# Kernel tuning notes

Hardware: AMD Instinct MI355X
Metric: run time of the kernel (lower is better)

Reference implementation:

```python
import jax, jax.numpy as jnp
import numpy as np

B, A, F, H = 64, 128, 32, 64


def setup_inputs() -> dict:
    key = jax.random.key(0)
    ks = jax.random.split(key, 16)
    def dense(k, fan_in, fan_out):
        return jax.random.normal(k, (fan_in, fan_out), jnp.float32) / np.sqrt(fan_in)
    inp = {
        "X": jax.random.normal(ks[0], (B, A, F), jnp.float32),
        "mask": jax.random.randint(ks[1], (B, A), 0, 2, jnp.int32),
        # base MLP: F -> H -> H -> 1
        "base_W1": dense(ks[2], F, H), "base_b1": jnp.zeros((H,), jnp.float32),
        "base_W2": dense(ks[3], H, H), "base_b2": jnp.zeros((H,), jnp.float32),
        "base_W3": dense(ks[4], H, 1), "base_b3": jnp.zeros((1,), jnp.float32),
        # pair MLP: 2F -> H -> H -> 1
        "pair_W1": dense(ks[5], 2 * F, H), "pair_b1": jnp.zeros((H,), jnp.float32),
        "pair_W2": dense(ks[6], H, H), "pair_b2": jnp.zeros((H,), jnp.float32),
        "pair_W3": dense(ks[7], H, 1), "pair_b3": jnp.zeros((1,), jnp.float32),
    }
    return inp


def reference(X, mask, base_W1, base_b1, base_W2, base_b2, base_W3, base_b3,
              pair_W1, pair_b1, pair_W2, pair_b2, pair_W3, pair_b3):
    f = X.shape[-1]
    a = X.shape[1]
    # base utility f_base(x_i): (B,A)
    hb = jax.nn.relu(jnp.einsum('baf,fh->bah', X, base_W1) + base_b1)
    hb = jax.nn.relu(jnp.einsum('bah,hk->bak', hb, base_W2) + base_b2)
    base_u = (jnp.einsum('bah,ho->bao', hb, base_W3) + base_b3)[..., 0]
    # pairwise MLP on concat([x_i, x_j]); first layer decomposed to avoid
    # materializing the (B,A,A,2F) concat: W1 = [Wi; Wj]
    Wi, Wj = pair_W1[:f], pair_W1[f:]
    hi = jnp.einsum('baf,fh->bah', X, Wi)  # contribution of x_i
    hj = jnp.einsum('baf,fh->bah', X, Wj)  # contribution of x_j
    h = jax.nn.relu(hi[:, :, None, :] + hj[:, None, :, :] + pair_b1)  # (B,A,A,H)
    h = jax.nn.relu(jnp.einsum('bijh,hk->bijk', h, pair_W2) + pair_b2)
    pe = (jnp.einsum('bijh,ho->bijo', h, pair_W3) + pair_b3)[..., 0]  # (B,A,A)
    # zero out diagonal (j != i)
    pe = pe * (1.0 - jnp.eye(a, dtype=pe.dtype))
    # availability mask on both i and j
    mf = mask.astype(pe.dtype)
    pe = pe * (mf[:, :, None] * mf[:, None, :])
    utilities = base_u + jnp.sum(pe, axis=-1)
    utilities = jnp.where(mask.astype(bool), utilities, jnp.float32(-1e9))
    return jax.nn.softmax(utilities, axis=-1)
```

## Files before the change

kernel.cpp:

```cpp
#include <hip/hip_runtime.h>
#include <hip/hip_bf16.h>

#define BB 64
#define AA 128
#define FF 32
#define HH 64
#define GXDIM 12

typedef float  f32x4  __attribute__((ext_vector_type(4)));
typedef float  f32x16 __attribute__((ext_vector_type(16)));
typedef __bf16 bf16x8 __attribute__((ext_vector_type(8)));
typedef unsigned int uint4v __attribute__((ext_vector_type(4)));

#define OFF_HIP   0
#define OFF_HJ    524288
#define OFF_BU    1048576
#define OFF_UTIL  1056768
#define OFF_W2FH  1064960
#define OFF_W2FL  1067008
#define OFF_JLIST 1069056
#define OFF_JCNT  1077248

static __device__ __forceinline__ unsigned short f2b_rne(float x) {
    __hip_bfloat16 h = __float2bfloat16(x);
    return __builtin_bit_cast(unsigned short, h);
}
static __device__ __forceinline__ float b2f(unsigned short u) {
    unsigned v = ((unsigned)u) << 16;
    return __builtin_bit_cast(float, v);
}

__global__ __launch_bounds__(64)
void ddc_features(const float* __restrict__ X, const int* __restrict__ mask,
                  const float* __restrict__ bW1, const float* __restrict__ bb1,
                  const float* __restrict__ bW2, const float* __restrict__ bb2,
                  const float* __restrict__ bW3, const float* __restrict__ bb3,
                  const float* __restrict__ pW1, const float* __restrict__ pb1,
                  const float* __restrict__ pW2,
                  float* __restrict__ hi_p, float* __restrict__ hj,
                  float* __restrict__ base_u,
                  unsigned short* __restrict__ W2fh,
                  unsigned short* __restrict__ W2fl,
                  int* __restrict__ jlist, int* __restrict__ jcnt) {
    const int a = blockIdx.x, b = blockIdx.y, lane = threadIdx.x;
    const int row = b * AA + a;

    const float* __restrict__ x = X + row * FF;
    float xr[FF];
#pragma unroll
    for (int f = 0; f < FF; ++f) xr[f] = x[f];

    float vhi = pb1[lane];
    float vhj = 0.f;
    float v1  = bb1[lane];
#pragma unroll
    for (int f = 0; f < FF; ++f) {
        vhi = fmaf(xr[f], pW1[f * HH + lane], vhi);
        vhj = fmaf(xr[f], pW1[(FF + f) * HH + lane], vhj);
        v1  = fmaf(xr[f], bW1[f * HH + lane], v1);
    }
    v1 = fmaxf(v1, 0.f);

    float v2 = bb2[lane];
#pragma unroll
    for (int k = 0; k < HH; ++k) {
        float hk = __shfl(v1, k);
        v2 = fmaf(hk, bW2[k * HH + lane], v2);
    }
    v2 = fmaxf(v2, 0.f);

    float bu = v2 * bW3[lane];
#pragma unroll
    for (int off = 32; off; off >>= 1) bu += __shfl_xor(bu, off);

    hi_p[row * HH + lane] = vhi;
    hj  [row * HH + lane] = vhj;
    if (lane == 0) base_u[row] = bu + bb3[0];

    if (a == 0) {
        int base0 = 0;
#pragma unroll
        for (int hlf = 0; hlf < 2; ++hlf) {
            int idx = hlf * 64 + lane;
            int m = mask[b * AA + idx];
            unsigned long long bal = __ballot(m != 0);
            int pos = __popcll(bal & ((1ull << lane) - 1ull));
            if (m) jlist[b * AA + base0 + pos] = idx;
            base0 += (int)__popcll(bal);
        }
        if (lane == 0) jcnt[b] = base0;
    }

    if (a == 1 && b == 0) {
        const int col = lane & 31, half = lane >> 5;
#pragma unroll
        for (int fid = 0; fid < 8; ++fid) {
            const int nt = fid >> 2, ks = fid & 3;
            const int n = nt * 32 + col;
            const int ko = ks * 16 + half * 8;
#pragma unroll
            for (int e = 0; e < 8; ++e) {
                float w = pW2[(ko + e) * HH + n];
                unsigned short uh = f2b_rne(w);
                W2fh[(fid * 64 + lane) * 8 + e] = uh;
                W2fl[(fid * 64 + lane) * 8 + e] = f2b_rne(w - b2f(uh));
            }
        }
    }
}

#define SPLIT_PAIR(pa, pb, outh, outl)                                   \
    {   unsigned ua = __builtin_bit_cast(unsigned, pa);                  \
        unsigned ub = __builtin_bit_cast(unsigned, pb);                  \
        outh = (ua >> 16) | (ub & 0xFFFF0000u);                          \
        float ra = pa - __builtin_bit_cast(float, ua & 0xFFFF0000u);     \
        float rb = pb - __builtin_bit_cast(float, ub & 0xFFFF0000u);     \
        unsigned va = __builtin_bit_cast(unsigned, ra);                  \
        unsigned vb = __builtin_bit_cast(unsigned, rb);                  \
        outl = (va >> 16) | (vb & 0xFFFF0000u); }

__global__ __launch_bounds__(256, 3)
void ddc_pairs_mfma(const float* __restrict__ hi_p, const float* __restrict__ hj,
                    const float* __restrict__ base_u,
                    const int* __restrict__ jlist, const int* __restrict__ jcnt,
                    const unsigned short* __restrict__ W2fh,
                    const unsigned short* __restrict__ W2fl,
                    const float* __restrict__ pb2, const float* __restrict__ pW3,
                    const float* __restrict__ pb3, float* __restrict__ util) {
    __shared__ float  sHJ[AA][HH + 4];
    __shared__ uint4v sBH[512];
    __shared__ uint4v sBL[512];

    const int t  = threadIdx.x;
    const int gx = blockIdx.x;
    const int b  = blockIdx.y;
    const int cnt = jcnt[b];
    const int ngroups = (cnt + 3) >> 2;
    if (gx >= ngroups) return;

    const int l = t & 63, wid = t >> 6;
    const int col = l & 31, half = l >> 5;

    {
        const uint4v* __restrict__ gbh = (const uint4v*)W2fh;
        const uint4v* __restrict__ gbl = (const uint4v*)W2fl;
        sBH[t]       = gbh[t];
        sBH[t + 256] = gbh[t + 256];
        sBL[t]       = gbl[t];
        sBL[t + 256] = gbl[t + 256];
    }

    {
        const int r = t >> 1, hf = t & 1;
        f32x4* dst = (f32x4*)&sHJ[r][hf * 32];
        if (r < cnt) {
            const int jr = jlist[b * AA + r];
            const f32x4* __restrict__ src =
                (const f32x4*)(hj + (b * AA + jr) * HH + hf * 32);
#pragma unroll
            for (int q = 0; q < 8; ++q) dst[q] = src[q];
        } else {
#pragma unroll
            for (int q = 0; q < 8; ++q) dst[q] = (f32x4)0.f;
        }
    }

    __syncthreads();

    const float b2v0 = pb2[col], b2v1 = pb2[32 + col];
    const float w3v0 = pW3[col], w3v1 = pW3[32 + col];
    const float b3s  = pb3[0] * (1.f / 32.f);

    const int ntiles = (cnt + 31) >> 5;

    for (int g = gx; g < ngroups; g += GXDIM) {
        const int slot = g * 4 + wid;
        if (slot >= cnt) continue;
        const int i = __builtin_amdgcn_readfirstlane(jlist[b * AA + slot]);

        const float* __restrict__ hp = hi_p + (b * AA + i) * HH;
        f32x4 yv[8];
#pragma unroll
        for (int ks = 0; ks < 4; ++ks) {
            const int ko = ks * 16 + half * 8;
            yv[2 * ks]     = *(const f32x4*)(hp + ko);
            yv[2 * ks + 1] = *(const f32x4*)(hp + ko + 4);
        }

        float tsum = 0.f;
        for (int jt = 0; jt < ntiles; ++jt) {
            unsigned zofs = 0;
            asm volatile("" : "+v"(zofs));

            f32x16 acc0 = b2v0, acc1 = b2v1;
            const int jj = jt * 32 + col;

#define KSTEP(ks)                                                           \
            {   const int ko = (ks) * 16 + half * 8;                        \
                uint4v bh0 = sBH[(ks) * 64 + l + zofs];                     \
                uint4v bl0 = sBL[(ks) * 64 + l + zofs];                     \
                uint4v bh1 = sBH[(4 + (ks)) * 64 + l + zofs];               \
                uint4v bl1 = sBL[(4 + (ks)) * 64 + l + zofs];               \
                f32x4 x0 = *(const f32x4*)&sHJ[jj][ko];                     \
                f32x4 x1 = *(const f32x4*)&sHJ[jj][ko + 4];                 \
                f32x4 y0 = yv[2 * (ks)], y1 = yv[2 * (ks) + 1];             \
                float h0 = fmaxf(x0[0] + y0[0], 0.f);                       \
                float h1 = fmaxf(x0[1] + y0[1], 0.f);                       \
                float h2 = fmaxf(x0[2] + y0[2], 0.f);                       \
                float h3 = fmaxf(x0[3] + y0[3], 0.f);                       \
                float h4 = fmaxf(x1[0] + y1[0], 0.f);                       \
                float h5 = fmaxf(x1[1] + y1[1], 0.f);                       \
                float h6 = fmaxf(x1[2] + y1[2], 0.f);                       \
                float h7 = fmaxf(x1[3] + y1[3], 0.f);                       \
                unsigned a01, a23, a45, a67, c01, c23, c45, c67;            \
                SPLIT_PAIR(h0, h1, a01, c01)                                \
                SPLIT_PAIR(h2, h3, a23, c23)                                \
                SPLIT_PAIR(h4, h5, a45, c45)                                \
                SPLIT_PAIR(h6, h7, a67, c67)                                \
                uint4v ahv = {a01, a23, a45, a67};                          \
                uint4v alv = {c01, c23, c45, c67};                          \
                bf16x8 ah = __builtin_bit_cast(bf16x8, ahv);                \
                bf16x8 al = __builtin_bit_cast(bf16x8, alv);                \
                acc0 = __builtin_amdgcn_mfma_f32_32x32x16_bf16(             \
                    al, __builtin_bit_cast(bf16x8, bh0), acc0, 0, 0, 0);    \
                acc1 = __builtin_amdgcn_mfma_f32_32x32x16_bf16(             \
                    al, __builtin_bit_cast(bf16x8, bh1), acc1, 0, 0, 0);    \
                acc0 = __builtin_amdgcn_mfma_f32_32x32x16_bf16(             \
                    ah, __builtin_bit_cast(bf16x8, bl0), acc0, 0, 0, 0);    \
                acc1 = __builtin_amdgcn_mfma_f32_32x32x16_bf16(             \
                    ah, __builtin_bit_cast(bf16x8, bl1), acc1, 0, 0, 0);    \
                acc0 = __builtin_amdgcn_mfma_f32_32x32x16_bf16(             \
                    ah, __builtin_bit_cast(bf16x8, bh0), acc0, 0, 0, 0);    \
                acc1 = __builtin_amdgcn_mfma_f32_32x32x16_bf16(             \
                    ah, __builtin_bit_cast(bf16x8, bh1), acc1, 0, 0, 0);    \
            }
            KSTEP(0)
            KSTEP(1)
            KSTEP(2)
            KSTEP(3)
#undef KSTEP

#pragma unroll
            for (int r = 0; r < 16; ++r) {
                const int rrow = (r & 3) + 8 * (r >> 2) + 4 * half;
                const int jg = jt * 32 + rrow;
                float v = fmaxf(acc0[r], 0.f) * w3v0 +
                          fmaxf(acc1[r], 0.f) * w3v1 + b3s;
                const bool valid = (jg < cnt) && (jg != slot);
                tsum += valid ? v : 0.f;
            }
        }
#pragma unroll
        for (int off = 32; off; off >>= 1) tsum += __shfl_xor(tsum, off);
        if (l == 0) util[b * AA + i] = base_u[b * AA + i] + tsum;
    }
}

__global__ __launch_bounds__(64)
void ddc_softmax(const float* __restrict__ util, const int* __restrict__ mask,
                 float* __restrict__ out) {
    const int b = blockIdx.x, lane = threadIdx.x;
    const int r0 = b * AA + lane, r1 = r0 + 64;
    const float u0 = (mask[r0] != 0) ? util[r0] : -1e9f;
    const float u1 = (mask[r1] != 0) ? util[r1] : -1e9f;

    float m = fmaxf(u0, u1);
#pragma unroll
    for (int off = 32; off; off >>= 1) m = fmaxf(m, __shfl_xor(m, off));

    const float e0 = __expf(u0 - m);
    const float e1 = __expf(u1 - m);
    float s = e0 + e1;
#pragma unroll
    for (int off = 32; off; off >>= 1) s += __shfl_xor(s, off);

    const float inv = 1.f / s;
    out[r0] = e0 * inv;
    out[r1] = e1 * inv;
}

extern "C" void kernel_launch(void* const* d_in, const int* in_sizes, int n_in,
                              void* d_out, int out_size, void* d_ws, size_t ws_size,
                              hipStream_t stream) {
    const float* X    = (const float*)d_in[0];
    const int*   mask = (const int*)  d_in[1];
    const float* bW1  = (const float*)d_in[2];
    const float* bb1  = (const float*)d_in[3];
    const float* bW2  = (const float*)d_in[4];
    const float* bb2  = (const float*)d_in[5];
    const float* bW3  = (const float*)d_in[6];
    const float* bb3  = (const float*)d_in[7];
    const float* pW1  = (const float*)d_in[8];
    const float* pb1  = (const float*)d_in[9];
    const float* pW2  = (const float*)d_in[10];
    const float* pb2  = (const float*)d_in[11];
    const float* pW3  = (const float*)d_in[12];
    const float* pb3  = (const float*)d_in[13];

    float* ws    = (float*)d_ws;
    float* hi_p  = ws + OFF_HIP;
    float* hjW   = ws + OFF_HJ;
    float* baseu = ws + OFF_BU;
    float* util  = ws + OFF_UTIL;
    unsigned short* W2fh = (unsigned short*)(ws + OFF_W2FH);
    unsigned short* W2fl = (unsigned short*)(ws + OFF_W2FL);
    int*   jlist = (int*)(ws + OFF_JLIST);
    int*   jcnt  = (int*)(ws + OFF_JCNT);

    float* out = (float*)d_out;

    dim3 g1(AA, BB);
    ddc_features<<<g1, 64, 0, stream>>>(X, mask, bW1, bb1, bW2, bb2, bW3, bb3,
                                        pW1, pb1, pW2,
                                        hi_p, hjW, baseu, W2fh, W2fl,
                                        jlist, jcnt);
    dim3 g2(GXDIM, BB);
    ddc_pairs_mfma<<<g2, 256, 0, stream>>>(hi_p, hjW, baseu, jlist, jcnt,
                                           W2fh, W2fl, pb2, pW3, pb3, util);
    ddc_softmax<<<BB, 64, 0, stream>>>(util, mask, out);
}
```

Before: 37.97 us.

## Fuse softmax into pair kernel via last-block counter and pack feature blocks

Removes the separate softmax launch: each pair block increments a per-batch atomic counter after writing utilities, and the last block for that batch computes the masked softmax. The feature kernel now runs four rows per 256-thread block instead of one row per 64-thread block, and it resets the counters. The pair kernel also skips zero-filling shared rows past the last used tile, and forces at least one group so batches with an empty mask still produce output. This saves one launch and some block scheduling overhead, at the cost of atomics, fences and a counter that must be reset on every call.

```diff
diff --git a/kernel.cpp b/kernel.cpp
--- a/kernel.cpp
+++ b/kernel.cpp
@@ -20,6 +20,7 @@
 #define OFF_W2FL  1067008
 #define OFF_JLIST 1069056
 #define OFF_JCNT  1077248
+#define OFF_BCTR  1077312
 
 static __device__ __forceinline__ unsigned short f2b_rne(float x) {
     __hip_bfloat16 h = __float2bfloat16(x);
@@ -30,7 +31,7 @@
     return __builtin_bit_cast(float, v);
 }
 
-__global__ __launch_bounds__(64)
+__global__ __launch_bounds__(256)
 void ddc_features(const float* __restrict__ X, const int* __restrict__ mask,
                   const float* __restrict__ bW1, const float* __restrict__ bb1,
                   const float* __restrict__ bW2, const float* __restrict__ bb2,
@@ -41,8 +42,11 @@
                   float* __restrict__ base_u,
                   unsigned short* __restrict__ W2fh,
                   unsigned short* __restrict__ W2fl,
-                  int* __restrict__ jlist, int* __restrict__ jcnt) {
-    const int a = blockIdx.x, b = blockIdx.y, lane = threadIdx.x;
+                  int* __restrict__ jlist, int* __restrict__ jcnt,
+                  int* __restrict__ bctr) {
+    const int t = threadIdx.x;
+    const int lane = t & 63, w = t >> 6;
+    const int a = blockIdx.x * 4 + w, b = blockIdx.y;
     const int row = b * AA + a;
 
     const float* __restrict__ x = X + row * FF;
@@ -100,13 +104,15 @@
             const int ko = ks * 16 + half * 8;
 #pragma unroll
             for (int e = 0; e < 8; ++e) {
-                float w = pW2[(ko + e) * HH + n];
-                unsigned short uh = f2b_rne(w);
+                float wv = pW2[(ko + e) * HH + n];
+                unsigned short uh = f2b_rne(wv);
                 W2fh[(fid * 64 + lane) * 8 + e] = uh;
-                W2fl[(fid * 64 + lane) * 8 + e] = f2b_rne(w - b2f(uh));
+                W2fl[(fid * 64 + lane) * 8 + e] = f2b_rne(wv - b2f(uh));
             }
         }
     }
+
+    if (a == 2 && b == 0) bctr[lane] = 0;
 }
 
 #define SPLIT_PAIR(pa, pb, outh, outl)                                   \
@@ -121,25 +127,30 @@
 
 __global__ __launch_bounds__(256, 3)
 void ddc_pairs_mfma(const float* __restrict__ hi_p, const float* __restrict__ hj,
-                    const float* __restrict__ base_u,
+                    const float* __restrict__ base_u, const int* __restrict__ mask,
                     const int* __restrict__ jlist, const int* __restrict__ jcnt,
                     const unsigned short* __restrict__ W2fh,
                     const unsigned short* __restrict__ W2fl,
                     const float* __restrict__ pb2, const float* __restrict__ pW3,
-                    const float* __restrict__ pb3, float* __restrict__ util) {
+                    const float* __restrict__ pb3, float* __restrict__ util,
+                    int* __restrict__ bctr, float* __restrict__ out) {
     __shared__ float  sHJ[AA][HH + 4];
     __shared__ uint4v sBH[512];
     __shared__ uint4v sBL[512];
+    __shared__ int sLast;
 
     const int t  = threadIdx.x;
     const int gx = blockIdx.x;
     const int b  = blockIdx.y;
     const int cnt = jcnt[b];
-    const int ngroups = (cnt + 3) >> 2;
+    int ngroups = (cnt + 3) >> 2;
+    if (ngroups == 0) ngroups = 1;
     if (gx >= ngroups) return;
 
     const int l = t & 63, wid = t >> 6;
     const int col = l & 31, half = l >> 5;
+    const int ntiles = (cnt + 31) >> 5;
+    const int rmax = ntiles << 5;
 
     {
         const uint4v* __restrict__ gbh = (const uint4v*)W2fh;
@@ -152,16 +163,18 @@
 
     {
         const int r = t >> 1, hf = t & 1;
-        f32x4* dst = (f32x4*)&sHJ[r][hf * 32];
-        if (r < cnt) {
-            const int jr = jlist[b * AA + r];
-            const f32x4* __restrict__ src =
-                (const f32x4*)(hj + (b * AA + jr) * HH + hf * 32);
-#pragma unroll
-            for (int q = 0; q < 8; ++q) dst[q] = src[q];
-        } else {
-#pragma unroll
-            for (int q = 0; q < 8; ++q) dst[q] = (f32x4)0.f;
+        if (r < rmax) {
+            f32x4* dst = (f32x4*)&sHJ[r][hf * 32];
+            if (r < cnt) {
+                const int jr = jlist[b * AA + r];
+                const f32x4* __restrict__ src =
+                    (const f32x4*)(hj + (b * AA + jr) * HH + hf * 32);
+#pragma unroll
+                for (int q = 0; q < 8; ++q) dst[q] = src[q];
+            } else {
+#pragma unroll
+                for (int q = 0; q < 8; ++q) dst[q] = (f32x4)0.f;
+            }
         }
     }
 
@@ -170,8 +183,6 @@
     const float b2v0 = pb2[col], b2v1 = pb2[32 + col];
     const float w3v0 = pW3[col], w3v1 = pW3[32 + col];
     const float b3s  = pb3[0] * (1.f / 32.f);
-
-    const int ntiles = (cnt + 31) >> 5;
 
     for (int g = gx; g < ngroups; g += GXDIM) {
         const int slot = g * 4 + wid;
@@ -254,29 +265,32 @@
         for (int off = 32; off; off >>= 1) tsum += __shfl_xor(tsum, off);
         if (l == 0) util[b * AA + i] = base_u[b * AA + i] + tsum;
     }
-}
-
-__global__ __launch_bounds__(64)
-void ddc_softmax(const float* __restrict__ util, const int* __restrict__ mask,
-                 float* __restrict__ out) {
-    const int b = blockIdx.x, lane = threadIdx.x;
-    const int r0 = b * AA + lane, r1 = r0 + 64;
-    const float u0 = (mask[r0] != 0) ? util[r0] : -1e9f;
-    const float u1 = (mask[r1] != 0) ? util[r1] : -1e9f;
-
-    float m = fmaxf(u0, u1);
-#pragma unroll
-    for (int off = 32; off; off >>= 1) m = fmaxf(m, __shfl_xor(m, off));
-
-    const float e0 = __expf(u0 - m);
-    const float e1 = __expf(u1 - m);
-    float s = e0 + e1;
-#pragma unroll
-    for (int off = 32; off; off >>= 1) s += __shfl_xor(s, off);
-
-    const float inv = 1.f / s;
-    out[r0] = e0 * inv;
-    out[r1] = e1 * inv;
+
+    __syncthreads();
+    if (t == 0) {
+        __threadfence();
+        const int nact = (ngroups < GXDIM) ? ngroups : GXDIM;
+        const int old = atomicAdd(&bctr[b], 1);
+        sLast = (old == nact - 1) ? 1 : 0;
+    }
+    __syncthreads();
+    if (sLast && t < 64) {
+        __threadfence();
+        const int r0 = b * AA + t, r1 = r0 + 64;
+        const float u0 = (mask[r0] != 0) ? util[r0] : -1e9f;
+        const float u1 = (mask[r1] != 0) ? util[r1] : -1e9f;
+        float m = fmaxf(u0, u1);
+#pragma unroll
+        for (int off = 32; off; off >>= 1) m = fmaxf(m, __shfl_xor(m, off));
+        const float e0 = __expf(u0 - m);
+        const float e1 = __expf(u1 - m);
+        float s = e0 + e1;
+#pragma unroll
+        for (int off = 32; off; off >>= 1) s += __shfl_xor(s, off);
+        const float inv = 1.f / s;
+        out[r0] = e0 * inv;
+        out[r1] = e1 * inv;
+    }
 }
 
 extern "C" void kernel_launch(void* const* d_in, const int* in_sizes, int n_in,
@@ -306,16 +320,17 @@
     unsigned short* W2fl = (unsigned short*)(ws + OFF_W2FL);
     int*   jlist = (int*)(ws + OFF_JLIST);
     int*   jcnt  = (int*)(ws + OFF_JCNT);
+    int*   bctr  = (int*)(ws + OFF_BCTR);
 
     float* out = (float*)d_out;
 
-    dim3 g1(AA, BB);
-    ddc_features<<<g1, 64, 0, stream>>>(X, mask, bW1, bb1, bW2, bb2, bW3, bb3,
-                                        pW1, pb1, pW2,
-                                        hi_p, hjW, baseu, W2fh, W2fl,
-                                        jlist, jcnt);
+    dim3 g1(AA / 4, BB);
+    ddc_features<<<g1, 256, 0, stream>>>(X, mask, bW1, bb1, bW2, bb2, bW3, bb3,
+                                         pW1, pb1, pW2,
+                                         hi_p, hjW, baseu, W2fh, W2fl,
+                                         jlist, jcnt, bctr);
     dim3 g2(GXDIM, BB);
-    ddc_pairs_mfma<<<g2, 256, 0, stream>>>(hi_p, hjW, baseu, jlist, jcnt,
-                                           W2fh, W2fl, pb2, pW3, pb3, util);
-    ddc_softmax<<<BB, 64, 0, stream>>>(util, mask, out);
-}
+    ddc_pairs_mfma<<<g2, 256, 0, stream>>>(hi_p, hjW, baseu, mask, jlist, jcnt,
+                                           W2fh, W2fl, pb2, pW3, pb3, util,
+                                           bctr, out);
+}
```

After: 50.54 us. 1.33x slower.

## Read W2 fragments and hi rows from global per tile to raise occupancy

Applied to the files above, without the earlier changes.

Drops the shared-memory staging of the bf16 hi/lo W2 fragments and the per-row register cache of hi, and reloads both from global memory (through cache) inside each j-tile step. The goal is lower LDS and VGPR use so that four blocks per CU fit, along with a wider grid in x (16 instead of 12 blocks per batch). In exchange every KSTEP issues extra global loads that depend on cache hits, where it used to read LDS or registers, which could add latency to the MFMA inner loop.

```diff
diff --git a/kernel.cpp b/kernel.cpp
--- a/kernel.cpp
+++ b/kernel.cpp
@@ -5,7 +5,7 @@
 #define AA 128
 #define FF 32
 #define HH 64
-#define GXDIM 12
+#define GXDIM 16
 
 typedef float  f32x4  __attribute__((ext_vector_type(4)));
 typedef float  f32x16 __attribute__((ext_vector_type(16)));
@@ -100,10 +100,10 @@
             const int ko = ks * 16 + half * 8;
 #pragma unroll
             for (int e = 0; e < 8; ++e) {
-                float w = pW2[(ko + e) * HH + n];
-                unsigned short uh = f2b_rne(w);
+                float wv = pW2[(ko + e) * HH + n];
+                unsigned short uh = f2b_rne(wv);
                 W2fh[(fid * 64 + lane) * 8 + e] = uh;
-                W2fl[(fid * 64 + lane) * 8 + e] = f2b_rne(w - b2f(uh));
+                W2fl[(fid * 64 + lane) * 8 + e] = f2b_rne(wv - b2f(uh));
             }
         }
     }
@@ -119,7 +119,7 @@
         unsigned vb = __builtin_bit_cast(unsigned, rb);                  \
         outl = (va >> 16) | (vb & 0xFFFF0000u); }
 
-__global__ __launch_bounds__(256, 3)
+__global__ __launch_bounds__(256, 4)
 void ddc_pairs_mfma(const float* __restrict__ hi_p, const float* __restrict__ hj,
                     const float* __restrict__ base_u,
                     const int* __restrict__ jlist, const int* __restrict__ jcnt,
@@ -127,9 +127,7 @@
                     const unsigned short* __restrict__ W2fl,
                     const float* __restrict__ pb2, const float* __restrict__ pW3,
                     const float* __restrict__ pb3, float* __restrict__ util) {
-    __shared__ float  sHJ[AA][HH + 4];
-    __shared__ uint4v sBH[512];
-    __shared__ uint4v sBL[512];
+    __shared__ float sHJ[AA][HH + 4];
 
     const int t  = threadIdx.x;
     const int gx = blockIdx.x;
@@ -140,15 +138,6 @@
 
     const int l = t & 63, wid = t >> 6;
     const int col = l & 31, half = l >> 5;
-
-    {
-        const uint4v* __restrict__ gbh = (const uint4v*)W2fh;
-        const uint4v* __restrict__ gbl = (const uint4v*)W2fl;
-        sBH[t]       = gbh[t];
-        sBH[t + 256] = gbh[t + 256];
-        sBL[t]       = gbl[t];
-        sBL[t + 256] = gbl[t + 256];
-    }
 
     {
         const int r = t >> 1, hf = t & 1;
@@ -177,15 +166,7 @@
         const int slot = g * 4 + wid;
         if (slot >= cnt) continue;
         const int i = __builtin_amdgcn_readfirstlane(jlist[b * AA + slot]);
-
         const float* __restrict__ hp = hi_p + (b * AA + i) * HH;
-        f32x4 yv[8];
-#pragma unroll
-        for (int ks = 0; ks < 4; ++ks) {
-            const int ko = ks * 16 + half * 8;
-            yv[2 * ks]     = *(const f32x4*)(hp + ko);
-            yv[2 * ks + 1] = *(const f32x4*)(hp + ko + 4);
-        }
 
         float tsum = 0.f;
         for (int jt = 0; jt < ntiles; ++jt) {
@@ -197,13 +178,18 @@
 
 #define KSTEP(ks)                                                           \
             {   const int ko = (ks) * 16 + half * 8;                        \
-                uint4v bh0 = sBH[(ks) * 64 + l + zofs];                     \
-                uint4v bl0 = sBL[(ks) * 64 + l + zofs];                     \
-                uint4v bh1 = sBH[(4 + (ks)) * 64 + l + zofs];               \
-                uint4v bl1 = sBL[(4 + (ks)) * 64 + l + zofs];               \
+                uint4v bh0 = *(const uint4v*)                               \
+                    (W2fh + ((ks) * 64 + l) * 8 + zofs);                    \
+                uint4v bl0 = *(const uint4v*)                               \
+                    (W2fl + ((ks) * 64 + l) * 8 + zofs);                    \
+                uint4v bh1 = *(const uint4v*)                               \
+                    (W2fh + ((4 + (ks)) * 64 + l) * 8 + zofs);              \
+                uint4v bl1 = *(const uint4v*)                               \
+                    (W2fl + ((4 + (ks)) * 64 + l) * 8 + zofs);              \
+                f32x4 y0 = *(const f32x4*)(hp + ko + zofs);                 \
+                f32x4 y1 = *(const f32x4*)(hp + ko + 4 + zofs);             \
                 f32x4 x0 = *(const f32x4*)&sHJ[jj][ko];                     \
                 f32x4 x1 = *(const f32x4*)&sHJ[jj][ko + 4];                 \
-                f32x4 y0 = yv[2 * (ks)], y1 = yv[2 * (ks) + 1];             \
                 float h0 = fmaxf(x0[0] + y0[0], 0.f);                       \
                 float h1 = fmaxf(x0[1] + y0[1], 0.f);                       \
                 float h2 = fmaxf(x0[2] + y0[2], 0.f);                       \
```

Result: slower. 62.36 us (+64.2%).

## Process two query rows per wave to reuse B fragments and sHJ loads

Applied to the files above, without the earlier changes.

Each wave now handles two i-slots at once, sharing the LDS-loaded W2 fragments and hj tile reads across both rows and interleaving independent MFMA chains. The grid is shrunk to match (8 slots per group, GXDIM 8), and the occupancy hint drops from 3 to 2 blocks per SM to leave room for the doubled accumulators. The aim is fewer LDS reads per MFMA and better MFMA pipelining, at the cost of register pressure, lower occupancy and fewer blocks in the grid.

```diff
diff --git a/kernel.cpp b/kernel.cpp
--- a/kernel.cpp
+++ b/kernel.cpp
@@ -5,7 +5,7 @@
 #define AA 128
 #define FF 32
 #define HH 64
-#define GXDIM 12
+#define GXDIM 8
 
 typedef float  f32x4  __attribute__((ext_vector_type(4)));
 typedef float  f32x16 __attribute__((ext_vector_type(16)));
@@ -100,10 +100,10 @@
             const int ko = ks * 16 + half * 8;
 #pragma unroll
             for (int e = 0; e < 8; ++e) {
-                float w = pW2[(ko + e) * HH + n];
-                unsigned short uh = f2b_rne(w);
+                float wv = pW2[(ko + e) * HH + n];
+                unsigned short uh = f2b_rne(wv);
                 W2fh[(fid * 64 + lane) * 8 + e] = uh;
-                W2fl[(fid * 64 + lane) * 8 + e] = f2b_rne(w - b2f(uh));
+                W2fl[(fid * 64 + lane) * 8 + e] = f2b_rne(wv - b2f(uh));
             }
         }
     }
@@ -119,7 +119,7 @@
         unsigned vb = __builtin_bit_cast(unsigned, rb);                  \
         outl = (va >> 16) | (vb & 0xFFFF0000u); }
 
-__global__ __launch_bounds__(256, 3)
+__global__ __launch_bounds__(256, 2)
 void ddc_pairs_mfma(const float* __restrict__ hi_p, const float* __restrict__ hj,
                     const float* __restrict__ base_u,
                     const int* __restrict__ jlist, const int* __restrict__ jcnt,
@@ -135,7 +135,7 @@
     const int gx = blockIdx.x;
     const int b  = blockIdx.y;
     const int cnt = jcnt[b];
-    const int ngroups = (cnt + 3) >> 2;
+    const int ngroups = (cnt + 7) >> 3;
     if (gx >= ngroups) return;
 
     const int l = t & 63, wid = t >> 6;
@@ -174,26 +174,54 @@
     const int ntiles = (cnt + 31) >> 5;
 
     for (int g = gx; g < ngroups; g += GXDIM) {
-        const int slot = g * 4 + wid;
-        if (slot >= cnt) continue;
-        const int i = __builtin_amdgcn_readfirstlane(jlist[b * AA + slot]);
-
-        const float* __restrict__ hp = hi_p + (b * AA + i) * HH;
-        f32x4 yv[8];
+        const int slot0 = g * 8 + wid * 2;
+        if (slot0 >= cnt) continue;
+        const int slot1 = slot0 + 1;
+        const bool has1 = (slot1 < cnt);
+        const int i0 = __builtin_amdgcn_readfirstlane(jlist[b * AA + slot0]);
+        const int i1 = has1 ?
+            __builtin_amdgcn_readfirstlane(jlist[b * AA + slot1]) : i0;
+
+        const float* __restrict__ hpA = hi_p + (b * AA + i0) * HH;
+        const float* __restrict__ hpB = hi_p + (b * AA + i1) * HH;
+        f32x4 yvA[8], yvB[8];
 #pragma unroll
         for (int ks = 0; ks < 4; ++ks) {
             const int ko = ks * 16 + half * 8;
-            yv[2 * ks]     = *(const f32x4*)(hp + ko);
-            yv[2 * ks + 1] = *(const f32x4*)(hp + ko + 4);
-        }
-
-        float tsum = 0.f;
+            yvA[2 * ks]     = *(const f32x4*)(hpA + ko);
+            yvA[2 * ks + 1] = *(const f32x4*)(hpA + ko + 4);
+            yvB[2 * ks]     = *(const f32x4*)(hpB + ko);
+            yvB[2 * ks + 1] = *(const f32x4*)(hpB + ko + 4);
+        }
+
+        float tsumA = 0.f, tsumB = 0.f;
         for (int jt = 0; jt < ntiles; ++jt) {
             unsigned zofs = 0;
             asm volatile("" : "+v"(zofs));
 
-            f32x16 acc0 = b2v0, acc1 = b2v1;
+            f32x16 accA0 = b2v0, accA1 = b2v1;
+            f32x16 accB0 = b2v0, accB1 = b2v1;
             const int jj = jt * 32 + col;
+
+#define BUILD_A(Y0, Y1, AH, AL)                                             \
+            bf16x8 AH, AL;                                                  \
+            {   float h0 = fmaxf(x0[0] + (Y0)[0], 0.f);                     \
+                float h1 = fmaxf(x0[1] + (Y0)[1], 0.f);                     \
+                float h2 = fmaxf(x0[2] + (Y0)[2], 0.f);                     \
+                float h3 = fmaxf(x0[3] + (Y0)[3], 0.f);                     \
+                float h4 = fmaxf(x1[0] + (Y1)[0], 0.f);                     \
+                float h5 = fmaxf(x1[1] + (Y1)[1], 0.f);                     \
+                float h6 = fmaxf(x1[2] + (Y1)[2], 0.f);                     \
+                float h7 = fmaxf(x1[3] + (Y1)[3], 0.f);                     \
+                unsigned a01, a23, a45, a67, c01, c23, c45, c67;            \
+                SPLIT_PAIR(h0, h1, a01, c01)                                \
+                SPLIT_PAIR(h2, h3, a23, c23)                                \
+                SPLIT_PAIR(h4, h5, a45, c45)                                \
+                SPLIT_PAIR(h6, h7, a67, c67)                                \
+                uint4v ahv = {a01, a23, a45, a67};                          \
+                uint4v alv = {c01, c23, c45, c67};                          \
+                AH = __builtin_bit_cast(bf16x8, ahv);                       \
+                AL = __builtin_bit_cast(bf16x8, alv); }
 
 #define KSTEP(ks)                                                           \
             {   const int ko = (ks) * 16 + half * 8;                        \
@@ -203,56 +231,55 @@
                 uint4v bl1 = sBL[(4 + (ks)) * 64 + l + zofs];               \
                 f32x4 x0 = *(const f32x4*)&sHJ[jj][ko];                     \
                 f32x4 x1 = *(const f32x4*)&sHJ[jj][ko + 4];                 \
-                f32x4 y0 = yv[2 * (ks)], y1 = yv[2 * (ks) + 1];             \
-                float h0 = fmaxf(x0[0] + y0[0], 0.f);                       \
-                float h1 = fmaxf(x0[1] + y0[1], 0.f);                       \
-                float h2 = fmaxf(x0[2] + y0[2], 0.f);                       \
-                float h3 = fmaxf(x0[3] + y0[3], 0.f);                       \
-                float h4 = fmaxf(x1[0] + y1[0], 0.f);                       \
-                float h5 = fmaxf(x1[1] + y1[1], 0.f);                       \
-                float h6 = fmaxf(x1[2] + y1[2], 0.f);                       \
-                float h7 = fmaxf(x1[3] + y1[3], 0.f);                       \
-                unsigned a01, a23, a45, a67, c01, c23, c45, c67;            \
-                SPLIT_PAIR(h0, h1, a01, c01)                                \
-                SPLIT_PAIR(h2, h3, a23, c23)                                \
-                SPLIT_PAIR(h4, h5, a45, c45)                                \
-                SPLIT_PAIR(h6, h7, a67, c67)                                \
-                uint4v ahv = {a01, a23, a45, a67};                          \
-                uint4v alv = {c01, c23, c45, c67};                          \
-                bf16x8 ah = __builtin_bit_cast(bf16x8, ahv);                \
-                bf16x8 al = __builtin_bit_cast(bf16x8, alv);                \
-                acc0 = __builtin_amdgcn_mfma_f32_32x32x16_bf16(             \
-                    al, __builtin_bit_cast(bf16x8, bh0), acc0, 0, 0, 0);    \
-                acc1 = __builtin_amdgcn_mfma_f32_32x32x16_bf16(             \
-                    al, __builtin_bit_cast(bf16x8, bh1), acc1, 0, 0, 0);    \
-                acc0 = __builtin_amdgcn_mfma_f32_32x32x16_bf16(             \
-                    ah, __builtin_bit_cast(bf16x8, bl0), acc0, 0, 0, 0);    \
-                acc1 = __builtin_amdgcn_mfma_f32_32x32x16_bf16(             \
-                    ah, __builtin_bit_cast(bf16x8, bl1), acc1, 0, 0, 0);    \
-                acc0 = __builtin_amdgcn_mfma_f32_32x32x16_bf16(             \
-                    ah, __builtin_bit_cast(bf16x8, bh0), acc0, 0, 0, 0);    \
-                acc1 = __builtin_amdgcn_mfma_f32_32x32x16_bf16(             \
-                    ah, __builtin_bit_cast(bf16x8, bh1), acc1, 0, 0, 0);    \
+                BUILD_A(yvA[2 * (ks)], yvA[2 * (ks) + 1], ahA, alA)         \
+                BUILD_A(yvB[2 * (ks)], yvB[2 * (ks) + 1], ahB, alB)         \
+                bf16x8 BH0 = __builtin_bit_cast(bf16x8, bh0);               \
+                bf16x8 BL0 = __builtin_bit_cast(bf16x8, bl0);               \
+                bf16x8 BH1 = __builtin_bit_cast(bf16x8, bh1);               \
+                bf16x8 BL1 = __builtin_bit_cast(bf16x8, bl1);               \
+                accA0 = __builtin_amdgcn_mfma_f32_32x32x16_bf16(alA, BH0, accA0, 0, 0, 0); \
+                accB0 = __builtin_amdgcn_mfma_f32_32x32x16_bf16(alB, BH0, accB0, 0, 0, 0); \
+                accA1 = __builtin_amdgcn_mfma_f32_32x32x16_bf16(alA, BH1, accA1, 0, 0, 0); \
+                accB1 = __builtin_amdgcn_mfma_f32_32x32x16_bf16(alB, BH1, accB1, 0, 0, 0); \
+                accA0 = __builtin_amdgcn_mfma_f32_32x32x16_bf16(ahA, BL0, accA0, 0, 0, 0); \
+                accB0 = __builtin_amdgcn_mfma_f32_32x32x16_bf16(ahB, BL0, accB0, 0, 0, 0); \
+                accA1 = __builtin_amdgcn_mfma_f32_32x32x16_bf16(ahA, BL1, accA1, 0, 0, 0); \
+                accB1 = __builtin_amdgcn_mfma_f32_32x32x16_bf16(ahB, BL1, accB1, 0, 0, 0); \
+                accA0 = __builtin_amdgcn_mfma_f32_32x32x16_bf16(ahA, BH0, accA0, 0, 0, 0); \
+                accB0 = __builtin_amdgcn_mfma_f32_32x32x16_bf16(ahB, BH0, accB0, 0, 0, 0); \
+                accA1 = __builtin_amdgcn_mfma_f32_32x32x16_bf16(ahA, BH1, accA1, 0, 0, 0); \
+                accB1 = __builtin_amdgcn_mfma_f32_32x32x16_bf16(ahB, BH1, accB1, 0, 0, 0); \
             }
             KSTEP(0)
             KSTEP(1)
             KSTEP(2)
             KSTEP(3)
 #undef KSTEP
+#undef BUILD_A
 
 #pragma unroll
             for (int r = 0; r < 16; ++r) {
                 const int rrow = (r & 3) + 8 * (r >> 2) + 4 * half;
                 const int jg = jt * 32 + rrow;
-                float v = fmaxf(acc0[r], 0.f) * w3v0 +
-                          fmaxf(acc1[r], 0.f) * w3v1 + b3s;
-                const bool valid = (jg < cnt) && (jg != slot);
-                tsum += valid ? v : 0.f;
+                float vA = fmaxf(accA0[r], 0.f) * w3v0 +
+                           fmaxf(accA1[r], 0.f) * w3v1 + b3s;
+                float vB = fmaxf(accB0[r], 0.f) * w3v0 +
+                           fmaxf(accB1[r], 0.f) * w3v1 + b3s;
+                const bool vaA = (jg < cnt) && (jg != slot0);
+                const bool vaB = (jg < cnt) && (jg != slot1);
+                tsumA += vaA ? vA : 0.f;
+                tsumB += vaB ? vB : 0.f;
             }
         }
 #pragma unroll
-        for (int off = 32; off; off >>= 1) tsum += __shfl_xor(tsum, off);
-        if (l == 0) util[b * AA + i] = base_u[b * AA + i] + tsum;
+        for (int off = 32; off; off >>= 1) {
+            tsumA += __shfl_xor(tsumA, off);
+            tsumB += __shfl_xor(tsumB, off);
+        }
+        if (l == 0) {
+            util[b * AA + i0] = base_u[b * AA + i0] + tsumA;
+            if (has1) util[b * AA + i1] = base_u[b * AA + i1] + tsumB;
+        }
     }
 }
 
```

Result: slower. 45.11 us (+18.8%).
